# Performance work log

Measured on AMD Instinct MI355X. Metric: run time of the kernel, lower is better.

## Reference

```python
import jax, jax.numpy as jnp
import numpy as np

EPS = 1e-5

def layernorm(t, gamma, beta):
    mu = jnp.mean(t, axis=-1, keepdims=True)
    var = jnp.mean(jnp.square(t - mu), axis=-1, keepdims=True)
    return (t - mu) * jax.lax.rsqrt(var + EPS) * gamma + beta

def setup_inputs() -> dict:
    key = jax.random.key(0)
    ks = jax.random.split(key, 9)
    B, M, N, C, D = 4, 4096, 32, 256, 128
    x = jax.random.normal(ks[0], (B, M, C), dtype=jnp.float32)
    y = jax.random.normal(ks[1], (B, M, N, C), dtype=jnp.float32)
    z = jax.random.normal(ks[2], (B, M, N, 1), dtype=jnp.float32)
    s = 1.0 / np.sqrt(C)
    Wq = jax.random.normal(ks[3], (C, D), dtype=jnp.float32) * s
    bq = jnp.zeros((D,), dtype=jnp.float32)
    Wk = jax.random.normal(ks[4], (C, D), dtype=jnp.float32) * s
    bk = jnp.zeros((D,), dtype=jnp.float32)
    q_gamma = jnp.ones((C,), dtype=jnp.float32)
    q_beta = jnp.zeros((C,), dtype=jnp.float32)
    k_gamma = jnp.ones((C,), dtype=jnp.float32)
    k_beta = jnp.zeros((C,), dtype=jnp.float32)
    return {"x": x, "y": y, "z": z, "q_gamma": q_gamma, "q_beta": q_beta,
            "Wq": Wq, "bq": bq, "k_gamma": k_gamma, "k_beta": k_beta,
            "Wk": Wk, "bk": bk}

def reference(x, y, z, q_gamma, q_beta, Wq, bq, k_gamma, k_beta, Wk, bk):
    D = Wq.shape[1]
    scale = D ** (-0.5)
    q = layernorm(x, q_gamma, q_beta) @ Wq + bq          # (B, M, D)
    k = layernorm(y, k_gamma, k_beta) @ Wk + bk          # (B, M, N, D)
    # single query vs N keys per node: (B, M, N)
    dot = scale * jnp.einsum('bmd,bmnd->bmn', q, k)
    attn = jax.nn.softmax(dot, axis=-1)[..., None]       # (B, M, N, 1)
    a = jnp.sum(attn * z, axis=-2)                       # (B, M, 1)
    return a
```

## Files before the change

### kernel.cpp

```cpp
#include <hip/hip_runtime.h>
#include <math.h>

#define NROWS 16384
#define NN 32
#define NC 256
#define ND 128
#define RB 8
#define LNEPS 1e-5f
#define SCALE 0.08838834764831845f

typedef float vfloat4 __attribute__((ext_vector_type(4)));

#define OFF_MT   0
#define OFF_UVEC 65536
#define OFF_VV   65792
#define OFF_M1   66048
#define OFF_WG   66304
#define OFF_SCAL 66560

__global__ __launch_bounds__(256)
void ca_prep_a(const float* __restrict__ Wq, const float* __restrict__ Wk,
               const float* __restrict__ qg, const float* __restrict__ qb,
               const float* __restrict__ kg, float* __restrict__ ws) {
    __shared__ __align__(16) float wkrow[ND];
    __shared__ float red[8];
    const int j = blockIdx.x;
    const int c = threadIdx.x;
    const int lane = c & 63, wv = c >> 6;
    if (c < ND / 4) *(float4*)(wkrow + 4 * c) = *(const float4*)(Wk + j * ND + 4 * c);
    __syncthreads();
    float m = 0.f;
    #pragma unroll 8
    for (int d = 0; d < ND; d += 4) {
        const float4 wq4 = *(const float4*)(Wq + c * ND + d);
        const float4 wk4 = *(const float4*)(wkrow + d);
        m += wq4.x * wk4.x + wq4.y * wk4.y + wq4.z * wk4.z + wq4.w * wk4.w;
    }
    const float kgj = kg[j];
    const float mpp = kgj * qg[c] * m;
    ws[OFF_MT + c * NC + j] = mpp;
    atomicAdd(&ws[OFF_M1 + c], mpp);
    float a = mpp, b = kgj * m * qb[c];
    #pragma unroll
    for (int s = 1; s < 64; s <<= 1) { a += __shfl_xor(a, s, 64); b += __shfl_xor(b, s, 64); }
    if (lane == 0) { red[wv] = a; red[4 + wv] = b; }
    __syncthreads();
    if (c == 0) {
        ws[OFF_UVEC + j] = red[0] + red[1] + red[2] + red[3];
        ws[OFF_VV + j]   = red[4] + red[5] + red[6] + red[7];
    }
}

__global__ __launch_bounds__(256)
void ca_prep_b(const float* __restrict__ Wq, const float* __restrict__ Wk,
               const float* __restrict__ qg, const float* __restrict__ qb,
               const float* __restrict__ kg, const float* __restrict__ kb,
               const float* __restrict__ bq, const float* __restrict__ bk,
               float* __restrict__ ws) {
    __shared__ float h[ND];
    __shared__ float htmp[2][ND];
    __shared__ float red[16];
    const int t = threadIdx.x, lane = t & 63, wv = t >> 6;
    {
        const int d = t & (ND - 1), half = t >> 7;
        float s = 0.f;
        #pragma unroll 8
        for (int j = half * 128; j < half * 128 + 128; ++j) s += Wk[j * ND + d] * kb[j];
        htmp[half][d] = s;
    }
    __syncthreads();
    if (t < ND) h[t] = bk[t] + htmp[0][t] + htmp[1][t];
    __syncthreads();
    float vvj;
    {
        float s = 0.f;
        #pragma unroll 8
        for (int d = 0; d < ND; d += 4) {
            const float4 w4 = *(const float4*)(Wk + t * ND + d);
            const float4 b4 = *(const float4*)(bq + d);
            s += w4.x * b4.x + w4.y * b4.y + w4.z * b4.z + w4.w * b4.w;
        }
        vvj = ws[OFF_VV + t] + kg[t] * s;
        ws[OFF_VV + t] = vvj;
    }
    float w = 0.f;
    #pragma unroll 8
    for (int d = 0; d < ND; d += 4) {
        const float4 w4 = *(const float4*)(Wq + t * ND + d);
        w += w4.x * h[d] + w4.y * h[d + 1] + w4.z * h[d + 2] + w4.w * h[d + 3];
    }
    ws[OFF_WG + t] = qg[t] * w;
    float r0 = qg[t] * w;
    float r1 = qb[t] * w + ((t < ND) ? bq[t] * h[t] : 0.f);
    float r2 = ws[OFF_UVEC + t];
    float r3 = vvj;
    #pragma unroll
    for (int s = 1; s < 64; s <<= 1) {
        r0 += __shfl_xor(r0, s, 64); r1 += __shfl_xor(r1, s, 64);
        r2 += __shfl_xor(r2, s, 64); r3 += __shfl_xor(r3, s, 64);
    }
    if (lane == 0) { red[wv] = r0; red[4 + wv] = r1; red[8 + wv] = r2; red[12 + wv] = r3; }
    __syncthreads();
    if (t == 0) {
        ws[OFF_SCAL + 0] = red[0] + red[1] + red[2] + red[3];
        ws[OFF_SCAL + 1] = red[4] + red[5] + red[6] + red[7];
        ws[OFF_SCAL + 2] = red[8] + red[9] + red[10] + red[11];
        ws[OFF_SCAL + 3] = red[12] + red[13] + red[14] + red[15];
    }
}

__global__ __launch_bounds__(256)
void ca_main(const float* __restrict__ x, const float* __restrict__ y,
             const float* __restrict__ z, const float* __restrict__ ws,
             float* __restrict__ out) {
    __shared__ __align__(16) float xs[RB * NC];
    __shared__ __align__(16) float tp[4 * RB * NC];
    const int tid = threadIdx.x;
    const int lane = tid & 63;
    const int wv = tid >> 6;
    const int row0 = blockIdx.x * RB;

    float mu_[2], rstd_[2], cst_[2], sgr_[2];

    {
        const float4 wg4 = *(const float4*)(ws + OFF_WG + 4 * lane);
        const float4 m14 = *(const float4*)(ws + OFF_M1 + 4 * lane);
        const float s0 = ws[OFF_SCAL + 0], s1c = ws[OFF_SCAL + 1];
        const float s2c = ws[OFF_SCAL + 2], s3c = ws[OFF_SCAL + 3];
        #pragma unroll
        for (int jj = 0; jj < 2; ++jj) {
            const int r = 2 * wv + jj;
            const float4 x4 = *(const float4*)(x + (size_t)(row0 + r) * NC + 4 * lane);
            *(float4*)(xs + r * NC + 4 * lane) = x4;
            float a = (x4.x + x4.y) + (x4.z + x4.w);
            float b = x4.x * x4.x + x4.y * x4.y + x4.z * x4.z + x4.w * x4.w;
            float cw = x4.x * wg4.x + x4.y * wg4.y + x4.z * wg4.z + x4.w * wg4.w;
            float dm = x4.x * m14.x + x4.y * m14.y + x4.z * m14.z + x4.w * m14.w;
            #pragma unroll
            for (int s = 1; s < 64; s <<= 1) {
                a += __shfl_xor(a, s, 64); b += __shfl_xor(b, s, 64);
                cw += __shfl_xor(cw, s, 64); dm += __shfl_xor(dm, s, 64);
            }
            const float mu = a * (1.f / NC);
            const float var = b * (1.f / NC) - mu * mu;
            const float rstd = rsqrtf(var + LNEPS);
            mu_[jj] = mu; rstd_[jj] = rstd;
            cst_[jj] = rstd * (cw - mu * s0) + s1c;
            sgr_[jj] = rstd * (dm - mu * s2c) + s3c;
        }
    }
    __syncthreads();

    {
        float acc[RB][4];
        #pragma unroll
        for (int r = 0; r < RB; ++r) { acc[r][0] = acc[r][1] = acc[r][2] = acc[r][3] = 0.f; }
        const float* Mt = ws + OFF_MT;
        const int cb = 64 * wv;
        #pragma unroll 2
        for (int cc = 0; cc < 64; cc += 4) {
            const int c = cb + cc;
            const float4 m0  = *(const float4*)(Mt + (c + 0) * NC + 4 * lane);
            const float4 m1v = *(const float4*)(Mt + (c + 1) * NC + 4 * lane);
            const float4 m2  = *(const float4*)(Mt + (c + 2) * NC + 4 * lane);
            const float4 m3  = *(const float4*)(Mt + (c + 3) * NC + 4 * lane);
            #pragma unroll
            for (int r = 0; r < RB; ++r) {
                const float4 xv = *(const float4*)(xs + r * NC + c);
                acc[r][0] = fmaf(xv.x, m0.x, fmaf(xv.y, m1v.x, fmaf(xv.z, m2.x, fmaf(xv.w, m3.x, acc[r][0]))));
                acc[r][1] = fmaf(xv.x, m0.y, fmaf(xv.y, m1v.y, fmaf(xv.z, m2.y, fmaf(xv.w, m3.y, acc[r][1]))));
                acc[r][2] = fmaf(xv.x, m0.z, fmaf(xv.y, m1v.z, fmaf(xv.z, m2.z, fmaf(xv.w, m3.z, acc[r][2]))));
                acc[r][3] = fmaf(xv.x, m0.w, fmaf(xv.y, m1v.w, fmaf(xv.z, m2.w, fmaf(xv.w, m3.w, acc[r][3]))));
            }
        }
        #pragma unroll
        for (int r = 0; r < RB; ++r) {
            float4 o; o.x = acc[r][0]; o.y = acc[r][1]; o.z = acc[r][2]; o.w = acc[r][3];
            *(float4*)(tp + (wv * RB + r) * NC + 4 * lane) = o;
        }
    }
    __syncthreads();

    {
        const float4 u4 = *(const float4*)(ws + OFF_UVEC + 4 * lane);
        const float4 v4 = *(const float4*)(ws + OFF_VV + 4 * lane);
        #pragma unroll
        for (int jj = 0; jj < 2; ++jj) {
            const int r = 2 * wv + jj;
            const float4 t0 = *(const float4*)(tp + (0 * RB + r) * NC + 4 * lane);
            const float4 t1 = *(const float4*)(tp + (1 * RB + r) * NC + 4 * lane);
            const float4 t2 = *(const float4*)(tp + (2 * RB + r) * NC + 4 * lane);
            const float4 t3 = *(const float4*)(tp + (3 * RB + r) * NC + 4 * lane);
            const float rstd = rstd_[jj], mu = mu_[jj];
            float4 gp;
            gp.x = rstd * ((t0.x + t1.x + t2.x + t3.x) - mu * u4.x) + v4.x;
            gp.y = rstd * ((t0.y + t1.y + t2.y + t3.y) - mu * u4.y) + v4.y;
            gp.z = rstd * ((t0.z + t1.z + t2.z + t3.z) - mu * u4.z) + v4.z;
            gp.w = rstd * ((t0.w + t1.w + t2.w + t3.w) - mu * u4.w) + v4.w;
            *(float4*)(tp + r * NC + 4 * lane) = gp;
        }
    }

    {
        const int g = lane >> 4;
        const int i = lane & 15;
        const int sig = 8 * g + (lane & 7);
        #pragma unroll
        for (int jj = 0; jj < 2; ++jj) {
            const int r = 2 * wv + jj;
            const size_t row = (size_t)row0 + r;
            const float* gl = tp + r * NC + 4 * i;
            const float4 g0 = *(const float4*)(gl + 0);
            const float4 g1 = *(const float4*)(gl + 64);
            const float4 g2 = *(const float4*)(gl + 128);
            const float4 g3 = *(const float4*)(gl + 192);
            const float cst = cst_[jj], sg = sgr_[jj];
            const float* kb0 = y + row * (size_t)(NN * NC) + (8 * g) * NC + 4 * i;
            const float zv = z[row * NN + sig];
            float dv = 0.f;
            #pragma unroll 2
            for (int kk = 0; kk < 8; ++kk) {
                const float* kp = kb0 + kk * NC;
                const vfloat4 y0 = __builtin_nontemporal_load((const vfloat4*)(kp + 0));
                const vfloat4 y1 = __builtin_nontemporal_load((const vfloat4*)(kp + 64));
                const vfloat4 y2 = __builtin_nontemporal_load((const vfloat4*)(kp + 128));
                const vfloat4 y3 = __builtin_nontemporal_load((const vfloat4*)(kp + 192));
                float s1 = ((y0.x + y0.y) + (y0.z + y0.w)) + ((y1.x + y1.y) + (y1.z + y1.w))
                         + ((y2.x + y2.y) + (y2.z + y2.w)) + ((y3.x + y3.y) + (y3.z + y3.w));
                float s2 = y0.x * y0.x + y0.y * y0.y + y0.z * y0.z + y0.w * y0.w;
                s2 += y1.x * y1.x + y1.y * y1.y + y1.z * y1.z + y1.w * y1.w;
                s2 += y2.x * y2.x + y2.y * y2.y + y2.z * y2.z + y2.w * y2.w;
                s2 += y3.x * y3.x + y3.y * y3.y + y3.z * y3.z + y3.w * y3.w;
                float s3 = y0.x * g0.x + y0.y * g0.y + y0.z * g0.z + y0.w * g0.w;
                s3 += y1.x * g1.x + y1.y * g1.y + y1.z * g1.z + y1.w * g1.w;
                s3 += y2.x * g2.x + y2.y * g2.y + y2.z * g2.z + y2.w * g2.w;
                s3 += y3.x * g3.x + y3.y * g3.y + y3.z * g3.z + y3.w * g3.w;
                #pragma unroll
                for (int s = 1; s < 16; s <<= 1) {
                    s1 += __shfl_xor(s1, s, 64);
                    s2 += __shfl_xor(s2, s, 64);
                    s3 += __shfl_xor(s3, s, 64);
                }
                const float mun = s1 * (1.f / NC);
                const float varn = s2 * (1.f / NC) - mun * mun;
                const float rsd = rsqrtf(varn + LNEPS);
                const float dotv = SCALE * (rsd * (s3 - mun * sg) + cst);
                dv = ((lane & 7) == kk) ? dotv : dv;
            }
            float mx = dv;
            #pragma unroll
            for (int s = 1; s < 64; s <<= 1) mx = fmaxf(mx, __shfl_xor(mx, s, 64));
            const float e = __expf(dv - mx);
            float num = e * zv, den = e;
            #pragma unroll
            for (int s = 1; s < 64; s <<= 1) {
                num += __shfl_xor(num, s, 64);
                den += __shfl_xor(den, s, 64);
            }
            if (lane == 0) out[row] = num / den;
        }
    }
}

extern "C" void kernel_launch(void* const* d_in, const int* in_sizes, int n_in,
                              void* d_out, int out_size, void* d_ws, size_t ws_size,
                              hipStream_t stream) {
    const float* x  = (const float*)d_in[0];
    const float* y  = (const float*)d_in[1];
    const float* z  = (const float*)d_in[2];
    const float* qg = (const float*)d_in[3];
    const float* qb = (const float*)d_in[4];
    const float* Wq = (const float*)d_in[5];
    const float* bq = (const float*)d_in[6];
    const float* kg = (const float*)d_in[7];
    const float* kb = (const float*)d_in[8];
    const float* Wk = (const float*)d_in[9];
    const float* bk = (const float*)d_in[10];
    float* out = (float*)d_out;
    float* ws = (float*)d_ws;

    (void)hipMemsetAsync(ws + OFF_M1, 0, NC * sizeof(float), stream);
    ca_prep_a<<<NC, 256, 0, stream>>>(Wq, Wk, qg, qb, kg, ws);
    ca_prep_b<<<1, 256, 0, stream>>>(Wq, Wk, qg, qb, kg, kb, bq, bk, ws);
    ca_main<<<NROWS / RB, 256, 0, stream>>>(x, y, z, ws, out);
}
```

Before: 155.7 us.

## Software-pipeline key loads in main loop and drop atomic M1 accumulation

The per-key loop over 8 keys is fully unrolled with explicit staging, so several 1 KB key rows are in flight while partial sums of earlier rows are computed, and all shuffle reductions are batched at the end. This is meant to raise memory-level parallelism on the bandwidth-bound y stream. The M1 row sums move from atomics in prep_a to a plain row reduction in prep_b, which removes the memset launch. A launch-bounds occupancy hint is added, and the larger register footprint may cause spills or lower occupancy.

```diff
diff --git a/kernel.cpp b/kernel.cpp
--- a/kernel.cpp
+++ b/kernel.cpp
@@ -39,7 +39,6 @@
     const float kgj = kg[j];
     const float mpp = kgj * qg[c] * m;
     ws[OFF_MT + c * NC + j] = mpp;
-    atomicAdd(&ws[OFF_M1 + c], mpp);
     float a = mpp, b = kgj * m * qb[c];
     #pragma unroll
     for (int s = 1; s < 64; s <<= 1) { a += __shfl_xor(a, s, 64); b += __shfl_xor(b, s, 64); }
@@ -62,6 +61,16 @@
     __shared__ float red[16];
     const int t = threadIdx.x, lane = t & 63, wv = t >> 6;
     {
+        float s = 0.f;
+        const float* mrow = ws + OFF_MT + t * NC;
+        #pragma unroll 8
+        for (int j2 = 0; j2 < NC; j2 += 4) {
+            const float4 m4 = *(const float4*)(mrow + j2);
+            s += (m4.x + m4.y) + (m4.z + m4.w);
+        }
+        ws[OFF_M1 + t] = s;
+    }
+    {
         const int d = t & (ND - 1), half = t >> 7;
         float s = 0.f;
         #pragma unroll 8
@@ -109,7 +118,7 @@
     }
 }
 
-__global__ __launch_bounds__(256)
+__global__ __launch_bounds__(256, 4)
 void ca_main(const float* __restrict__ x, const float* __restrict__ y,
              const float* __restrict__ z, const float* __restrict__ ws,
              float* __restrict__ out) {
@@ -205,48 +214,69 @@
         const int g = lane >> 4;
         const int i = lane & 15;
         const int sig = 8 * g + (lane & 7);
-        #pragma unroll
         for (int jj = 0; jj < 2; ++jj) {
             const int r = 2 * wv + jj;
             const size_t row = (size_t)row0 + r;
             const float* gl = tp + r * NC + 4 * i;
-            const float4 g0 = *(const float4*)(gl + 0);
-            const float4 g1 = *(const float4*)(gl + 64);
-            const float4 g2 = *(const float4*)(gl + 128);
-            const float4 g3 = *(const float4*)(gl + 192);
+            const vfloat4 g0 = *(const vfloat4*)(gl + 0);
+            const vfloat4 g1 = *(const vfloat4*)(gl + 64);
+            const vfloat4 g2 = *(const vfloat4*)(gl + 128);
+            const vfloat4 g3 = *(const vfloat4*)(gl + 192);
             const float cst = cst_[jj], sg = sgr_[jj];
             const float* kb0 = y + row * (size_t)(NN * NC) + (8 * g) * NC + 4 * i;
             const float zv = z[row * NN + sig];
             float dv = 0.f;
-            #pragma unroll 2
-            for (int kk = 0; kk < 8; ++kk) {
-                const float* kp = kb0 + kk * NC;
-                const vfloat4 y0 = __builtin_nontemporal_load((const vfloat4*)(kp + 0));
-                const vfloat4 y1 = __builtin_nontemporal_load((const vfloat4*)(kp + 64));
-                const vfloat4 y2 = __builtin_nontemporal_load((const vfloat4*)(kp + 128));
-                const vfloat4 y3 = __builtin_nontemporal_load((const vfloat4*)(kp + 192));
-                float s1 = ((y0.x + y0.y) + (y0.z + y0.w)) + ((y1.x + y1.y) + (y1.z + y1.w))
-                         + ((y2.x + y2.y) + (y2.z + y2.w)) + ((y3.x + y3.y) + (y3.z + y3.w));
-                float s2 = y0.x * y0.x + y0.y * y0.y + y0.z * y0.z + y0.w * y0.w;
-                s2 += y1.x * y1.x + y1.y * y1.y + y1.z * y1.z + y1.w * y1.w;
-                s2 += y2.x * y2.x + y2.y * y2.y + y2.z * y2.z + y2.w * y2.w;
-                s2 += y3.x * y3.x + y3.y * y3.y + y3.z * y3.z + y3.w * y3.w;
-                float s3 = y0.x * g0.x + y0.y * g0.y + y0.z * g0.z + y0.w * g0.w;
-                s3 += y1.x * g1.x + y1.y * g1.y + y1.z * g1.z + y1.w * g1.w;
-                s3 += y2.x * g2.x + y2.y * g2.y + y2.z * g2.z + y2.w * g2.w;
-                s3 += y3.x * g3.x + y3.y * g3.y + y3.z * g3.z + y3.w * g3.w;
-                #pragma unroll
-                for (int s = 1; s < 16; s <<= 1) {
-                    s1 += __shfl_xor(s1, s, 64);
-                    s2 += __shfl_xor(s2, s, 64);
-                    s3 += __shfl_xor(s3, s, 64);
-                }
-                const float mun = s1 * (1.f / NC);
-                const float varn = s2 * (1.f / NC) - mun * mun;
-                const float rsd = rsqrtf(varn + LNEPS);
-                const float dotv = SCALE * (rsd * (s3 - mun * sg) + cst);
-                dv = ((lane & 7) == kk) ? dotv : dv;
+
+#define LOADK(K) \
+            const vfloat4 ya##K = __builtin_nontemporal_load((const vfloat4*)(kb0 + K * NC + 0)); \
+            const vfloat4 yb##K = __builtin_nontemporal_load((const vfloat4*)(kb0 + K * NC + 64)); \
+            const vfloat4 yc##K = __builtin_nontemporal_load((const vfloat4*)(kb0 + K * NC + 128)); \
+            const vfloat4 yd##K = __builtin_nontemporal_load((const vfloat4*)(kb0 + K * NC + 192));
+
+#define PARTK(K) \
+            float s1_##K = (((ya##K.x + ya##K.y) + (ya##K.z + ya##K.w)) + ((yb##K.x + yb##K.y) + (yb##K.z + yb##K.w))) \
+                         + (((yc##K.x + yc##K.y) + (yc##K.z + yc##K.w)) + ((yd##K.x + yd##K.y) + (yd##K.z + yd##K.w))); \
+            float s2_##K = ya##K.x*ya##K.x + ya##K.y*ya##K.y + ya##K.z*ya##K.z + ya##K.w*ya##K.w \
+                         + yb##K.x*yb##K.x + yb##K.y*yb##K.y + yb##K.z*yb##K.z + yb##K.w*yb##K.w \
+                         + yc##K.x*yc##K.x + yc##K.y*yc##K.y + yc##K.z*yc##K.z + yc##K.w*yc##K.w \
+                         + yd##K.x*yd##K.x + yd##K.y*yd##K.y + yd##K.z*yd##K.z + yd##K.w*yd##K.w; \
+            float s3_##K = ya##K.x*g0.x + ya##K.y*g0.y + ya##K.z*g0.z + ya##K.w*g0.w \
+                         + yb##K.x*g1.x + yb##K.y*g1.y + yb##K.z*g1.z + yb##K.w*g1.w \
+                         + yc##K.x*g2.x + yc##K.y*g2.y + yc##K.z*g2.z + yc##K.w*g2.w \
+                         + yd##K.x*g3.x + yd##K.y*g3.y + yd##K.z*g3.z + yd##K.w*g3.w;
+
+#define RED3K(K) \
+            _Pragma("unroll") \
+            for (int s = 1; s < 16; s <<= 1) { \
+                s1_##K += __shfl_xor(s1_##K, s, 64); \
+                s2_##K += __shfl_xor(s2_##K, s, 64); \
+                s3_##K += __shfl_xor(s3_##K, s, 64); \
             }
+
+#define EPIK(K) \
+            { const float mun = s1_##K * (1.f / NC); \
+              const float varn = s2_##K * (1.f / NC) - mun * mun; \
+              const float rsd = rsqrtf(varn + LNEPS); \
+              const float dt = SCALE * (rsd * (s3_##K - mun * sg) + cst); \
+              dv = ((lane & 7) == K) ? dt : dv; }
+
+            LOADK(0) LOADK(1) LOADK(2)
+            PARTK(0)
+            LOADK(3) PARTK(1)
+            LOADK(4) PARTK(2)
+            LOADK(5) PARTK(3)
+            LOADK(6) PARTK(4)
+            LOADK(7) PARTK(5)
+            PARTK(6) PARTK(7)
+            RED3K(0) RED3K(1) RED3K(2) RED3K(3)
+            RED3K(4) RED3K(5) RED3K(6) RED3K(7)
+            EPIK(0) EPIK(1) EPIK(2) EPIK(3)
+            EPIK(4) EPIK(5) EPIK(6) EPIK(7)
+#undef LOADK
+#undef PARTK
+#undef RED3K
+#undef EPIK
+
             float mx = dv;
             #pragma unroll
             for (int s = 1; s < 64; s <<= 1) mx = fmaxf(mx, __shfl_xor(mx, s, 64));
@@ -279,7 +309,6 @@
     float* out = (float*)d_out;
     float* ws = (float*)d_ws;
 
-    (void)hipMemsetAsync(ws + OFF_M1, 0, NC * sizeof(float), stream);
     ca_prep_a<<<NC, 256, 0, stream>>>(Wq, Wk, qg, qb, kg, ws);
     ca_prep_b<<<1, 256, 0, stream>>>(Wq, Wk, qg, qb, kg, kb, bq, bk, ws);
     ca_main<<<NROWS / RB, 256, 0, stream>>>(x, y, z, ws, out);
```

Result: slower. 219.6 us (+41.1%).

## Split main kernel into row-prep and y-streaming kernels via workspace

Applied to the files above, without the earlier changes.

Splits the fused main kernel in two. The first kernel computes the per-row projected query vector and scalars and writes them to a global workspace. The second kernel, which uses no shared memory, streams y and reads those values back, aiming at higher occupancy and better latency hiding on the bandwidth-bound y stream. The M1 atomic-plus-memset is replaced by a row sum in prep_b. The cost is an extra launch and a 16 MB round trip through global memory for the gp buffer.

```diff
diff --git a/kernel.cpp b/kernel.cpp
--- a/kernel.cpp
+++ b/kernel.cpp
@@ -17,6 +17,8 @@
 #define OFF_M1   66048
 #define OFF_WG   66304
 #define OFF_SCAL 66560
+#define OFF_GP   66816
+#define OFF_RS   (66816 + NROWS * NC)
 
 __global__ __launch_bounds__(256)
 void ca_prep_a(const float* __restrict__ Wq, const float* __restrict__ Wk,
@@ -39,7 +41,6 @@
     const float kgj = kg[j];
     const float mpp = kgj * qg[c] * m;
     ws[OFF_MT + c * NC + j] = mpp;
-    atomicAdd(&ws[OFF_M1 + c], mpp);
     float a = mpp, b = kgj * m * qb[c];
     #pragma unroll
     for (int s = 1; s < 64; s <<= 1) { a += __shfl_xor(a, s, 64); b += __shfl_xor(b, s, 64); }
@@ -62,6 +63,16 @@
     __shared__ float red[16];
     const int t = threadIdx.x, lane = t & 63, wv = t >> 6;
     {
+        float s = 0.f;
+        const float* mrow = ws + OFF_MT + t * NC;
+        #pragma unroll 8
+        for (int j2 = 0; j2 < NC; j2 += 4) {
+            const float4 m4 = *(const float4*)(mrow + j2);
+            s += (m4.x + m4.y) + (m4.z + m4.w);
+        }
+        ws[OFF_M1 + t] = s;
+    }
+    {
         const int d = t & (ND - 1), half = t >> 7;
         float s = 0.f;
         #pragma unroll 8
@@ -109,10 +120,8 @@
     }
 }
 
-__global__ __launch_bounds__(256)
-void ca_main(const float* __restrict__ x, const float* __restrict__ y,
-             const float* __restrict__ z, const float* __restrict__ ws,
-             float* __restrict__ out) {
+__global__ __launch_bounds__(256, 4)
+void ca_rowprep(const float* __restrict__ x, float* __restrict__ ws) {
     __shared__ __align__(16) float xs[RB * NC];
     __shared__ __align__(16) float tp[4 * RB * NC];
     const int tid = threadIdx.x;
@@ -120,7 +129,7 @@
     const int wv = tid >> 6;
     const int row0 = blockIdx.x * RB;
 
-    float mu_[2], rstd_[2], cst_[2], sgr_[2];
+    float mu_[2], rstd_[2];
 
     {
         const float4 wg4 = *(const float4*)(ws + OFF_WG + 4 * lane);
@@ -145,8 +154,11 @@
             const float var = b * (1.f / NC) - mu * mu;
             const float rstd = rsqrtf(var + LNEPS);
             mu_[jj] = mu; rstd_[jj] = rstd;
-            cst_[jj] = rstd * (cw - mu * s0) + s1c;
-            sgr_[jj] = rstd * (dm - mu * s2c) + s3c;
+            if (lane == 0) {
+                const size_t row = (size_t)(row0 + r);
+                ws[OFF_RS + row * 2 + 0] = rstd * (cw - mu * s0) + s1c;
+                ws[OFF_RS + row * 2 + 1] = rstd * (dm - mu * s2c) + s3c;
+            }
         }
     }
     __syncthreads();
@@ -197,68 +209,74 @@
             gp.y = rstd * ((t0.y + t1.y + t2.y + t3.y) - mu * u4.y) + v4.y;
             gp.z = rstd * ((t0.z + t1.z + t2.z + t3.z) - mu * u4.z) + v4.z;
             gp.w = rstd * ((t0.w + t1.w + t2.w + t3.w) - mu * u4.w) + v4.w;
-            *(float4*)(tp + r * NC + 4 * lane) = gp;
-        }
-    }
-
-    {
-        const int g = lane >> 4;
-        const int i = lane & 15;
-        const int sig = 8 * g + (lane & 7);
-        #pragma unroll
-        for (int jj = 0; jj < 2; ++jj) {
-            const int r = 2 * wv + jj;
-            const size_t row = (size_t)row0 + r;
-            const float* gl = tp + r * NC + 4 * i;
-            const float4 g0 = *(const float4*)(gl + 0);
-            const float4 g1 = *(const float4*)(gl + 64);
-            const float4 g2 = *(const float4*)(gl + 128);
-            const float4 g3 = *(const float4*)(gl + 192);
-            const float cst = cst_[jj], sg = sgr_[jj];
-            const float* kb0 = y + row * (size_t)(NN * NC) + (8 * g) * NC + 4 * i;
-            const float zv = z[row * NN + sig];
-            float dv = 0.f;
-            #pragma unroll 2
-            for (int kk = 0; kk < 8; ++kk) {
-                const float* kp = kb0 + kk * NC;
-                const vfloat4 y0 = __builtin_nontemporal_load((const vfloat4*)(kp + 0));
-                const vfloat4 y1 = __builtin_nontemporal_load((const vfloat4*)(kp + 64));
-                const vfloat4 y2 = __builtin_nontemporal_load((const vfloat4*)(kp + 128));
-                const vfloat4 y3 = __builtin_nontemporal_load((const vfloat4*)(kp + 192));
-                float s1 = ((y0.x + y0.y) + (y0.z + y0.w)) + ((y1.x + y1.y) + (y1.z + y1.w))
-                         + ((y2.x + y2.y) + (y2.z + y2.w)) + ((y3.x + y3.y) + (y3.z + y3.w));
-                float s2 = y0.x * y0.x + y0.y * y0.y + y0.z * y0.z + y0.w * y0.w;
-                s2 += y1.x * y1.x + y1.y * y1.y + y1.z * y1.z + y1.w * y1.w;
-                s2 += y2.x * y2.x + y2.y * y2.y + y2.z * y2.z + y2.w * y2.w;
-                s2 += y3.x * y3.x + y3.y * y3.y + y3.z * y3.z + y3.w * y3.w;
-                float s3 = y0.x * g0.x + y0.y * g0.y + y0.z * g0.z + y0.w * g0.w;
-                s3 += y1.x * g1.x + y1.y * g1.y + y1.z * g1.z + y1.w * g1.w;
-                s3 += y2.x * g2.x + y2.y * g2.y + y2.z * g2.z + y2.w * g2.w;
-                s3 += y3.x * g3.x + y3.y * g3.y + y3.z * g3.z + y3.w * g3.w;
-                #pragma unroll
-                for (int s = 1; s < 16; s <<= 1) {
-                    s1 += __shfl_xor(s1, s, 64);
-                    s2 += __shfl_xor(s2, s, 64);
-                    s3 += __shfl_xor(s3, s, 64);
-                }
-                const float mun = s1 * (1.f / NC);
-                const float varn = s2 * (1.f / NC) - mun * mun;
-                const float rsd = rsqrtf(varn + LNEPS);
-                const float dotv = SCALE * (rsd * (s3 - mun * sg) + cst);
-                dv = ((lane & 7) == kk) ? dotv : dv;
+            *(float4*)(ws + OFF_GP + (size_t)(row0 + r) * NC + 4 * lane) = gp;
+        }
+    }
+}
+
+__global__ __launch_bounds__(256)
+void ca_stream(const float* __restrict__ y, const float* __restrict__ z,
+               const float* __restrict__ ws, float* __restrict__ out) {
+    const int tid = threadIdx.x;
+    const int lane = tid & 63;
+    const int wv = tid >> 6;
+    const int row0 = blockIdx.x * RB;
+    const int g = lane >> 4;
+    const int i = lane & 15;
+    const int sig = 8 * g + (lane & 7);
+
+    for (int jj = 0; jj < 2; ++jj) {
+        const size_t row = (size_t)row0 + 2 * wv + jj;
+        const float* gl = ws + OFF_GP + row * NC + 4 * i;
+        const vfloat4 g0 = *(const vfloat4*)(gl + 0);
+        const vfloat4 g1 = *(const vfloat4*)(gl + 64);
+        const vfloat4 g2 = *(const vfloat4*)(gl + 128);
+        const vfloat4 g3 = *(const vfloat4*)(gl + 192);
+        const float cst = ws[OFF_RS + row * 2 + 0];
+        const float sg  = ws[OFF_RS + row * 2 + 1];
+        const float* kb0 = y + row * (size_t)(NN * NC) + (8 * g) * NC + 4 * i;
+        const float zv = z[row * NN + sig];
+        float dv = 0.f;
+        #pragma unroll 2
+        for (int kk = 0; kk < 8; ++kk) {
+            const float* kp = kb0 + kk * NC;
+            const vfloat4 y0 = __builtin_nontemporal_load((const vfloat4*)(kp + 0));
+            const vfloat4 y1 = __builtin_nontemporal_load((const vfloat4*)(kp + 64));
+            const vfloat4 y2 = __builtin_nontemporal_load((const vfloat4*)(kp + 128));
+            const vfloat4 y3 = __builtin_nontemporal_load((const vfloat4*)(kp + 192));
+            float s1 = ((y0.x + y0.y) + (y0.z + y0.w)) + ((y1.x + y1.y) + (y1.z + y1.w))
+                     + ((y2.x + y2.y) + (y2.z + y2.w)) + ((y3.x + y3.y) + (y3.z + y3.w));
+            float s2 = y0.x * y0.x + y0.y * y0.y + y0.z * y0.z + y0.w * y0.w;
+            s2 += y1.x * y1.x + y1.y * y1.y + y1.z * y1.z + y1.w * y1.w;
+            s2 += y2.x * y2.x + y2.y * y2.y + y2.z * y2.z + y2.w * y2.w;
+            s2 += y3.x * y3.x + y3.y * y3.y + y3.z * y3.z + y3.w * y3.w;
+            float s3 = y0.x * g0.x + y0.y * g0.y + y0.z * g0.z + y0.w * g0.w;
+            s3 += y1.x * g1.x + y1.y * g1.y + y1.z * g1.z + y1.w * g1.w;
+            s3 += y2.x * g2.x + y2.y * g2.y + y2.z * g2.z + y2.w * g2.w;
+            s3 += y3.x * g3.x + y3.y * g3.y + y3.z * g3.z + y3.w * g3.w;
+            #pragma unroll
+            for (int s = 1; s < 16; s <<= 1) {
+                s1 += __shfl_xor(s1, s, 64);
+                s2 += __shfl_xor(s2, s, 64);
+                s3 += __shfl_xor(s3, s, 64);
             }
-            float mx = dv;
-            #pragma unroll
-            for (int s = 1; s < 64; s <<= 1) mx = fmaxf(mx, __shfl_xor(mx, s, 64));
-            const float e = __expf(dv - mx);
-            float num = e * zv, den = e;
-            #pragma unroll
-            for (int s = 1; s < 64; s <<= 1) {
-                num += __shfl_xor(num, s, 64);
-                den += __shfl_xor(den, s, 64);
-            }
-            if (lane == 0) out[row] = num / den;
-        }
+            const float mun = s1 * (1.f / NC);
+            const float varn = s2 * (1.f / NC) - mun * mun;
+            const float rsd = rsqrtf(varn + LNEPS);
+            const float dotv = SCALE * (rsd * (s3 - mun * sg) + cst);
+            dv = ((lane & 7) == kk) ? dotv : dv;
+        }
+        float mx = dv;
+        #pragma unroll
+        for (int s = 1; s < 64; s <<= 1) mx = fmaxf(mx, __shfl_xor(mx, s, 64));
+        const float e = __expf(dv - mx);
+        float num = e * zv, den = e;
+        #pragma unroll
+        for (int s = 1; s < 64; s <<= 1) {
+            num += __shfl_xor(num, s, 64);
+            den += __shfl_xor(den, s, 64);
+        }
+        if (lane == 0) out[row] = num / den;
     }
 }
 
@@ -279,8 +297,8 @@
     float* out = (float*)d_out;
     float* ws = (float*)d_ws;
 
-    (void)hipMemsetAsync(ws + OFF_M1, 0, NC * sizeof(float), stream);
     ca_prep_a<<<NC, 256, 0, stream>>>(Wq, Wk, qg, qb, kg, ws);
     ca_prep_b<<<1, 256, 0, stream>>>(Wq, Wk, qg, qb, kg, kb, bq, bk, ws);
-    ca_main<<<NROWS / RB, 256, 0, stream>>>(x, y, z, ws, out);
-}
+    ca_rowprep<<<NROWS / RB, 256, 0, stream>>>(x, ws);
+    ca_stream<<<NROWS / RB, 256, 0, stream>>>(y, z, ws, out);
+}
```

Result: slower. 174.4 us (+12.0%).
